# Kernel optimization log

Measured on AMD Instinct MI355X. Metric: run time of the kernel, lower is better.

Reference implementation:

```python
import jax, jax.numpy as jnp
import numpy as np

# Biquad Butterworth low-pass (cutoff = Nyquist/2), matches init_kwargs b/a.
B_COEF = np.array([0.2929, 0.5858, 0.2929], dtype=np.float32)
A_COEF = np.array([1.0, 0.0, 0.1716], dtype=np.float32)


def setup_inputs() -> dict:
    key = jax.random.key(0)
    x = jax.random.normal(key, (512, 65536), dtype=jnp.float32)  # (batch, T)
    return {"x": x, "b": jnp.asarray(B_COEF), "a": jnp.asarray(A_COEF)}


def reference(x, b, a):
    """IIR digital filter: y[t] = (sum_m b[m] x[t-m] - sum_{n>=1} a[n] y[t-n]) / a[0].

    x: (B, T), b: (M+1,), a: (N+1,). Returns y: (B, T).
    """
    M1 = b.shape[0]          # M+1 numerator taps
    N = a.shape[0] - 1       # feedback order
    # Causal FIR (feedforward) part: u[t] = sum_m b[m] * x[t-m].
    # conv_general_dilated is cross-correlation, so flip b to get convolution.
    u = jax.lax.conv_general_dilated(
        x[:, None, :],                 # (B, 1, T)
        b[::-1][None, None, :],        # (1, 1, M+1)
        window_strides=(1,),
        padding=[(M1 - 1, 0)],         # causal left-pad
    )[:, 0, :]                         # (B, T)

    a0 = a[0]
    a_rest = a[1:]                     # (N,)
    Bsz = x.shape[0]

    def step(yprev, ut):
        # yprev: (N, B) with yprev[0] = y[t-1]; ut: (B,)
        yt = (ut - a_rest @ yprev) / a0            # (B,)
        yprev = jnp.concatenate([yt[None, :], yprev[:-1]], axis=0)
        return yprev, yt

    init = jnp.zeros((N, Bsz), dtype=x.dtype)
    _, ys = jax.lax.scan(step, init, u.T)          # ys: (T, B)
    return ys.T                                    # (B, T)
```

## Files before the change

kernel.cpp:

```cpp
#include <hip/hip_runtime.h>

#define T_LEN 65536
#define WSEG  1024
#define CHUNK 16
#define WARM  24
#define NT    256
#define NWAVE 4
#define TP    20

typedef float vfloat4 __attribute__((ext_vector_type(4)));

#define SQMAT(a00,a01,a10,a11) {                      \
    float n00=a00*a00+a01*a10, n01=a00*a01+a01*a11;   \
    float n10=a10*a00+a11*a10, n11=a10*a01+a11*a11;   \
    a00=n00; a01=n01; a10=n10; a11=n11; }

__attribute__((amdgpu_flat_work_group_size(NT, NT)))
__global__ void iir_wave_kernel(const float* __restrict__ x,
                                const float* __restrict__ bco,
                                const float* __restrict__ aco,
                                float* __restrict__ y)
{
    const int tid  = threadIdx.x;
    const int wave = tid >> 6;
    const int lane = tid & 63;
    const long segbase = (long)blockIdx.x * (NWAVE * WSEG) + (long)wave * WSEG;
    const long base    = segbase + (long)lane * CHUNK;
    const bool rowstart = ((segbase & (T_LEN - 1)) == 0);

    const float inv_a0 = 1.0f / aco[0];
    const float b0 = bco[0]*inv_a0, b1 = bco[1]*inv_a0, b2 = bco[2]*inv_a0;
    const float c1 = aco[1]*inv_a0, c2 = aco[2]*inv_a0;

    __shared__ float tbuf[NWAVE][64][TP];

    float4 wv0, wv1, wv2, wv3, wv4, wv5;
    if (!rowstart) {
        const float4* wv = (const float4*)(x + segbase - WARM);
        wv0 = wv[0]; wv1 = wv[1]; wv2 = wv[2];
        wv3 = wv[3]; wv4 = wv[4]; wv5 = wv[5];
    }

    const float4* xv = (const float4*)(x + base);
    float4 v0 = xv[0], v1 = xv[1], v2 = xv[2], v3 = xv[3];

    float fm1 = 0.f, fm2 = 0.f;
    float t0 = 0.f, t1 = 0.f;
    if (!rowstart) {
        float w1 = 0.f, w2 = 0.f;
        float4 wvv[6] = { wv0, wv1, wv2, wv3, wv4, wv5 };
        #pragma unroll
        for (int q = 0; q < WARM / 4; ++q) {
            float4 v = wvv[q];
            float u0 = b0*v.x + b1*fm1 + b2*fm2;
            float u1 = b0*v.y + b1*v.x + b2*fm1;
            float u2 = b0*v.z + b1*v.y + b2*v.x;
            float u3 = b0*v.w + b1*v.z + b2*v.y;
            fm2 = v.z; fm1 = v.w;
            float y0 = u0 - c1*w1 - c2*w2;
            float y1 = u1 - c1*y0 - c2*w1;
            float y2 = u2 - c1*y1 - c2*y0;
            float y3 = u3 - c1*y2 - c2*y1;
            w2 = y2; w1 = y3;
        }
        t0 = w1; t1 = w2;
    }

    float xm1 = __shfl_up(v3.w, 1, 64);
    float xm2 = __shfl_up(v3.z, 1, 64);
    if (lane == 0) { xm1 = fm1; xm2 = fm2; }

    float u[CHUNK];
    float yp1 = 0.f, yp2 = 0.f;
#define STEP4(V, O)                                                  \
    {                                                                \
        float u0 = b0*(V).x + b1*xm1   + b2*xm2;                     \
        float u1 = b0*(V).y + b1*(V).x + b2*xm1;                     \
        float u2 = b0*(V).z + b1*(V).y + b2*(V).x;                   \
        float u3 = b0*(V).w + b1*(V).z + b2*(V).y;                   \
        xm2 = (V).z; xm1 = (V).w;                                    \
        u[(O)+0]=u0; u[(O)+1]=u1; u[(O)+2]=u2; u[(O)+3]=u3;          \
        float y0 = u0 - c1*yp1 - c2*yp2;                             \
        float y1 = u1 - c1*y0  - c2*yp1;                             \
        float y2 = u2 - c1*y1  - c2*y0;                              \
        float y3 = u3 - c1*y2  - c2*y1;                              \
        yp2 = y2; yp1 = y3;                                          \
    }
    STEP4(v0, 0) STEP4(v1, 4) STEP4(v2, 8) STEP4(v3, 12)
#undef STEP4
    #pragma unroll
    for (int j = 0; j < CHUNK; ++j) asm volatile("" : "+v"(u[j]));

    float s0 = yp1, s1 = yp2;
    float m00 = -c1, m01 = -c2, m10 = 1.f, m11 = 0.f;
    #pragma unroll
    for (int k = 0; k < 4; ++k) SQMAT(m00,m01,m10,m11)
    #pragma unroll
    for (int k = 0; k < 6; ++k) {
        int off = 1 << k;
        float p0 = __shfl_up(s0, off, 64);
        float p1 = __shfl_up(s1, off, 64);
        if (lane < off) { p0 = 0.f; p1 = 0.f; }
        s0 += m00*p0 + m01*p1;
        s1 += m10*p0 + m11*p1;
        if (lane & off) {
            float q0 = m00*t0 + m01*t1;
            float q1 = m10*t0 + m11*t1;
            t0 = q0; t1 = q1;
        }
        SQMAT(m00,m01,m10,m11)
    }

    float ex0 = __shfl_up(s0, 1, 64);
    float ex1 = __shfl_up(s1, 1, 64);
    if (lane == 0) { ex0 = 0.f; ex1 = 0.f; }

    yp1 = ex0 + t0;
    yp2 = ex1 + t1;
    #pragma unroll
    for (int j = 0; j < CHUNK; ++j) {
        float yj = u[j] - c1*yp1 - c2*yp2;
        yp2 = yp1; yp1 = yj;
        u[j] = yj;
    }

    float* wb = &tbuf[wave][0][0];
    #pragma unroll
    for (int q = 0; q < 4; ++q)
        *(float4*)(wb + lane*TP + 4*q) = make_float4(u[4*q], u[4*q+1], u[4*q+2], u[4*q+3]);
    asm volatile("s_waitcnt lgkmcnt(0)" ::: "memory");
    __builtin_amdgcn_sched_barrier(0);
    __builtin_amdgcn_wave_barrier();

    #pragma unroll
    for (int i = 0; i < 4; ++i) {
        int idx = i * 256 + 4 * lane;
        int cc  = idx >> 4;
        int jj  = idx & 15;
        vfloat4 o;
        o.x = wb[cc*TP + jj + 0];
        o.y = wb[cc*TP + jj + 1];
        o.z = wb[cc*TP + jj + 2];
        o.w = wb[cc*TP + jj + 3];
        __builtin_nontemporal_store(o, (vfloat4*)(y + segbase + idx));
    }
}

extern "C" void kernel_launch(void* const* d_in, const int* in_sizes, int n_in,
                              void* d_out, int out_size, void* d_ws, size_t ws_size,
                              hipStream_t stream) {
    const float* x = (const float*)d_in[0];
    const float* b = (const float*)d_in[1];
    const float* a = (const float*)d_in[2];
    float* y = (float*)d_out;

    const int nblocks = in_sizes[0] / (NWAVE * WSEG);
    iir_wave_kernel<<<nblocks, NT, 0, stream>>>(x, b, a, y);
}
```

Baseline: 46.64 us.

## Process four consecutive segments per wave with carried state and prefetch

Each wave now handles four consecutive 1024-sample segments instead of one. The filter state and the last inputs are carried exactly from one segment to the next, so only the first segment needs the warm-up pass. Loads for the next segment are issued before the current one is computed, overlapping memory latency with the scan. The grid shrinks fourfold, which cuts warm-up work and launch parallelism but gives fewer waves to hide latency and adds a serial dependency across segments.

```diff
diff --git a/kernel.cpp b/kernel.cpp
--- a/kernel.cpp
+++ b/kernel.cpp
@@ -2,6 +2,7 @@
 
 #define T_LEN 65536
 #define WSEG  1024
+#define NSEG  4
 #define CHUNK 16
 #define WARM  24
 #define NT    256
@@ -15,6 +16,12 @@
     float n10=a10*a00+a11*a10, n11=a10*a01+a11*a11;   \
     a00=n00; a01=n01; a10=n10; a11=n11; }
 
+#define WAVE_FENCE() do {                                   \
+    asm volatile("s_waitcnt lgkmcnt(0)" ::: "memory");      \
+    __builtin_amdgcn_sched_barrier(0);                      \
+    __builtin_amdgcn_wave_barrier();                        \
+} while (0)
+
 __attribute__((amdgpu_flat_work_group_size(NT, NT)))
 __global__ void iir_wave_kernel(const float* __restrict__ x,
                                 const float* __restrict__ bco,
@@ -24,9 +31,8 @@
     const int tid  = threadIdx.x;
     const int wave = tid >> 6;
     const int lane = tid & 63;
-    const long segbase = (long)blockIdx.x * (NWAVE * WSEG) + (long)wave * WSEG;
-    const long base    = segbase + (long)lane * CHUNK;
-    const bool rowstart = ((segbase & (T_LEN - 1)) == 0);
+    const long wbase = (long)blockIdx.x * (NWAVE * NSEG * WSEG) + (long)wave * (NSEG * WSEG);
+    const bool rowstart = ((wbase & (T_LEN - 1)) == 0);
 
     const float inv_a0 = 1.0f / aco[0];
     const float b0 = bco[0]*inv_a0, b1 = bco[1]*inv_a0, b2 = bco[2]*inv_a0;
@@ -36,13 +42,13 @@
 
     float4 wv0, wv1, wv2, wv3, wv4, wv5;
     if (!rowstart) {
-        const float4* wv = (const float4*)(x + segbase - WARM);
+        const float4* wv = (const float4*)(x + wbase - WARM);
         wv0 = wv[0]; wv1 = wv[1]; wv2 = wv[2];
         wv3 = wv[3]; wv4 = wv[4]; wv5 = wv[5];
     }
 
-    const float4* xv = (const float4*)(x + base);
-    float4 v0 = xv[0], v1 = xv[1], v2 = xv[2], v3 = xv[3];
+    const float4* xv = (const float4*)(x + wbase + (long)lane * CHUNK);
+    float4 a0 = xv[0], a1 = xv[1], a2 = xv[2], a3 = xv[3];
 
     float fm1 = 0.f, fm2 = 0.f;
     float t0 = 0.f, t1 = 0.f;
@@ -66,83 +72,101 @@
         t0 = w1; t1 = w2;
     }
 
-    float xm1 = __shfl_up(v3.w, 1, 64);
-    float xm2 = __shfl_up(v3.z, 1, 64);
-    if (lane == 0) { xm1 = fm1; xm2 = fm2; }
-
-    float u[CHUNK];
-    float yp1 = 0.f, yp2 = 0.f;
-#define STEP4(V, O)                                                  \
-    {                                                                \
-        float u0 = b0*(V).x + b1*xm1   + b2*xm2;                     \
-        float u1 = b0*(V).y + b1*(V).x + b2*xm1;                     \
-        float u2 = b0*(V).z + b1*(V).y + b2*(V).x;                   \
-        float u3 = b0*(V).w + b1*(V).z + b2*(V).y;                   \
-        xm2 = (V).z; xm1 = (V).w;                                    \
-        u[(O)+0]=u0; u[(O)+1]=u1; u[(O)+2]=u2; u[(O)+3]=u3;          \
-        float y0 = u0 - c1*yp1 - c2*yp2;                             \
-        float y1 = u1 - c1*y0  - c2*yp1;                             \
-        float y2 = u2 - c1*y1  - c2*y0;                              \
-        float y3 = u3 - c1*y2  - c2*y1;                              \
-        yp2 = y2; yp1 = y3;                                          \
-    }
-    STEP4(v0, 0) STEP4(v1, 4) STEP4(v2, 8) STEP4(v3, 12)
-#undef STEP4
-    #pragma unroll
-    for (int j = 0; j < CHUNK; ++j) asm volatile("" : "+v"(u[j]));
-
-    float s0 = yp1, s1 = yp2;
-    float m00 = -c1, m01 = -c2, m10 = 1.f, m11 = 0.f;
-    #pragma unroll
-    for (int k = 0; k < 4; ++k) SQMAT(m00,m01,m10,m11)
-    #pragma unroll
-    for (int k = 0; k < 6; ++k) {
-        int off = 1 << k;
-        float p0 = __shfl_up(s0, off, 64);
-        float p1 = __shfl_up(s1, off, 64);
-        if (lane < off) { p0 = 0.f; p1 = 0.f; }
-        s0 += m00*p0 + m01*p1;
-        s1 += m10*p0 + m11*p1;
-        if (lane & off) {
-            float q0 = m00*t0 + m01*t1;
-            float q1 = m10*t0 + m11*t1;
-            t0 = q0; t1 = q1;
-        }
-        SQMAT(m00,m01,m10,m11)
-    }
-
-    float ex0 = __shfl_up(s0, 1, 64);
-    float ex1 = __shfl_up(s1, 1, 64);
-    if (lane == 0) { ex0 = 0.f; ex1 = 0.f; }
-
-    yp1 = ex0 + t0;
-    yp2 = ex1 + t1;
-    #pragma unroll
-    for (int j = 0; j < CHUNK; ++j) {
-        float yj = u[j] - c1*yp1 - c2*yp2;
-        yp2 = yp1; yp1 = yj;
-        u[j] = yj;
-    }
-
     float* wb = &tbuf[wave][0][0];
-    #pragma unroll
-    for (int q = 0; q < 4; ++q)
-        *(float4*)(wb + lane*TP + 4*q) = make_float4(u[4*q], u[4*q+1], u[4*q+2], u[4*q+3]);
-    asm volatile("s_waitcnt lgkmcnt(0)" ::: "memory");
-    __builtin_amdgcn_sched_barrier(0);
-    __builtin_amdgcn_wave_barrier();
 
     #pragma unroll
-    for (int i = 0; i < 4; ++i) {
-        int idx = i * 256 + 4 * lane;
-        int cc  = idx >> 4;
-        int jj  = idx & 15;
-        vfloat4 o;
-        o.x = wb[cc*TP + jj + 0];
-        o.y = wb[cc*TP + jj + 1];
-        o.z = wb[cc*TP + jj + 2];
-        o.w = wb[cc*TP + jj + 3];
-        __builtin_nontemporal_store(o, (vfloat4*)(y + segbase + idx));
+    for (int s = 0; s < NSEG; ++s) {
+        const long segbase = wbase + (long)s * WSEG;
+
+        float4 nb0, nb1, nb2, nb3;
+        if (s < NSEG - 1) {
+            const float4* nx = (const float4*)(x + segbase + WSEG + (long)lane * CHUNK);
+            nb0 = nx[0]; nb1 = nx[1]; nb2 = nx[2]; nb3 = nx[3];
+        }
+
+        float xm1 = __shfl_up(a3.w, 1, 64);
+        float xm2 = __shfl_up(a3.z, 1, 64);
+        if (lane == 0) { xm1 = fm1; xm2 = fm2; }
+
+        float u[CHUNK];
+        float yp1 = 0.f, yp2 = 0.f;
+#define STEP4(V, O)                                                  \
+        {                                                            \
+            float u0 = b0*(V).x + b1*xm1   + b2*xm2;                 \
+            float u1 = b0*(V).y + b1*(V).x + b2*xm1;                 \
+            float u2 = b0*(V).z + b1*(V).y + b2*(V).x;               \
+            float u3 = b0*(V).w + b1*(V).z + b2*(V).y;               \
+            xm2 = (V).z; xm1 = (V).w;                                \
+            u[(O)+0]=u0; u[(O)+1]=u1; u[(O)+2]=u2; u[(O)+3]=u3;      \
+            float y0 = u0 - c1*yp1 - c2*yp2;                         \
+            float y1 = u1 - c1*y0  - c2*yp1;                         \
+            float y2 = u2 - c1*y1  - c2*y0;                          \
+            float y3 = u3 - c1*y2  - c2*y1;                          \
+            yp2 = y2; yp1 = y3;                                      \
+        }
+        STEP4(a0, 0) STEP4(a1, 4) STEP4(a2, 8) STEP4(a3, 12)
+#undef STEP4
+        #pragma unroll
+        for (int j = 0; j < CHUNK; ++j) asm volatile("" : "+v"(u[j]));
+
+        float s0 = yp1, s1 = yp2;
+        float m00 = -c1, m01 = -c2, m10 = 1.f, m11 = 0.f;
+        #pragma unroll
+        for (int k = 0; k < 4; ++k) SQMAT(m00,m01,m10,m11)
+        #pragma unroll
+        for (int k = 0; k < 6; ++k) {
+            int off = 1 << k;
+            float p0 = __shfl_up(s0, off, 64);
+            float p1 = __shfl_up(s1, off, 64);
+            if (lane < off) { p0 = 0.f; p1 = 0.f; }
+            s0 += m00*p0 + m01*p1;
+            s1 += m10*p0 + m11*p1;
+            if (lane & off) {
+                float q0 = m00*t0 + m01*t1;
+                float q1 = m10*t0 + m11*t1;
+                t0 = q0; t1 = q1;
+            }
+            SQMAT(m00,m01,m10,m11)
+        }
+
+        float ex0 = __shfl_up(s0, 1, 64);
+        float ex1 = __shfl_up(s1, 1, 64);
+        if (lane == 0) { ex0 = 0.f; ex1 = 0.f; }
+
+        yp1 = ex0 + t0;
+        yp2 = ex1 + t1;
+        #pragma unroll
+        for (int j = 0; j < CHUNK; ++j) {
+            float yj = u[j] - c1*yp1 - c2*yp2;
+            yp2 = yp1; yp1 = yj;
+            u[j] = yj;
+        }
+
+        float ct0 = __shfl(yp1, 63, 64);
+        float ct1 = __shfl(yp2, 63, 64);
+        float cf1 = __shfl(a3.w, 63, 64);
+        float cf2 = __shfl(a3.z, 63, 64);
+
+        #pragma unroll
+        for (int q = 0; q < 4; ++q)
+            *(float4*)(wb + lane*TP + 4*q) = make_float4(u[4*q], u[4*q+1], u[4*q+2], u[4*q+3]);
+        WAVE_FENCE();
+        #pragma unroll
+        for (int i = 0; i < 4; ++i) {
+            int idx = i * 256 + 4 * lane;
+            int cc  = idx >> 4;
+            int jj  = idx & 15;
+            vfloat4 o;
+            o.x = wb[cc*TP + jj + 0];
+            o.y = wb[cc*TP + jj + 1];
+            o.z = wb[cc*TP + jj + 2];
+            o.w = wb[cc*TP + jj + 3];
+            __builtin_nontemporal_store(o, (vfloat4*)(y + segbase + idx));
+        }
+        WAVE_FENCE();
+
+        t0 = ct0; t1 = ct1; fm1 = cf1; fm2 = cf2;
+        a0 = nb0; a1 = nb1; a2 = nb2; a3 = nb3;
     }
 }
 
@@ -154,6 +178,6 @@
     const float* a = (const float*)d_in[2];
     float* y = (float*)d_out;
 
-    const int nblocks = in_sizes[0] / (NWAVE * WSEG);
+    const int nblocks = in_sizes[0] / (NWAVE * NSEG * WSEG);
     iir_wave_kernel<<<nblocks, NT, 0, stream>>>(x, b, a, y);
 }
```

Result: faster. 44.57 us (-4.4%).
